# Optimization experiments

Hardware: AMD Instinct MI355X
Metric: run time of the kernel (lower is better)

The kernel has to match this reference:

```python
import jax, jax.numpy as jnp
import numpy as np

B, S, HID, H, D = 4, 1024, 2048, 16, 128
ROT = D // 2  # GLM 2D rotary: rotary dim is half the head dim (64)


def _rope_tables(seq_len, dim, base=10000.0):
    # dim = ROT; inv_freq over dim//2 frequencies, emb = cat(freqs, freqs)
    inv_freq = 1.0 / (base ** (jnp.arange(0, dim, 2, dtype=jnp.float32) / dim))
    t = jnp.arange(seq_len, dtype=jnp.float32)
    freqs = jnp.einsum('s,f->sf', t, inv_freq)          # [S, dim//2]
    emb = jnp.concatenate([freqs, freqs], axis=-1)       # [S, dim]
    return jnp.cos(emb), jnp.sin(emb)


def _rotate_half(x):
    x1, x2 = jnp.split(x, 2, axis=-1)
    return jnp.concatenate([-x2, x1], axis=-1)


def _apply_rope(x, cos, sin, pos_id):
    # x: [B,H,S,ROT]; pos_id: [B,S]; tables: [S,ROT]
    c = cos[pos_id][:, None, :, :]  # [B,1,S,ROT]
    s = sin[pos_id][:, None, :, :]
    return x * c + _rotate_half(x) * s


def setup_inputs() -> dict:
    key = jax.random.key(0)
    ks = jax.random.split(key, 12)
    w = 0.02
    inp = {
        'query': jax.random.normal(ks[0], (B, S, HID), jnp.float32),
        'key': jax.random.normal(ks[1], (B, S, HID), jnp.float32),
        'value': jax.random.normal(ks[2], (B, S, HID), jnp.float32),
        'mask': jnp.zeros((B, 1, S, S), jnp.float32),
        'position_bias': jax.random.normal(ks[3], (1, H, S, S), jnp.float32) * 0.1,
        'prev_attn': jax.random.normal(ks[4], (B, H, S, S), jnp.float32) * 0.1,
        'position_ids': jax.random.randint(ks[5], (B, 2, S), 0, S, jnp.int32),
        'Wq': jax.random.normal(ks[6], (HID, HID), jnp.float32) * w,
        'bq': jnp.zeros((HID,), jnp.float32),
        'Wk': jax.random.normal(ks[7], (HID, HID), jnp.float32) * w,
        'bk': jnp.zeros((HID,), jnp.float32),
        'Wv': jax.random.normal(ks[8], (HID, HID), jnp.float32) * w,
        'bv': jnp.zeros((HID,), jnp.float32),
        'Wo': jax.random.normal(ks[9], (HID, HID), jnp.float32) * w,
        'bo': jnp.zeros((HID,), jnp.float32),
    }
    return inp


def reference(query, key, value, mask, position_bias, prev_attn,
              Wq, bq, Wk, bk, Wv, bv, Wo, bo, position_ids):
    # QKV projections -> [B,H,S,D]
    def proj(x, W, b):
        return (x @ W.T + b).reshape(B, S, H, D).transpose(0, 2, 1, 3)
    q = proj(query, Wq, bq)
    k = proj(key, Wk, bk)
    v = proj(value, Wv, bv)

    # GLM 2D rotary: split head dim in halves, rope each with its own ids
    q1, q2 = jnp.split(q, 2, axis=-1)
    k1, k2 = jnp.split(k, 2, axis=-1)
    cos, sin = _rope_tables(S, ROT)
    pid = position_ids[:, 0, :]        # [B,S]
    bid = position_ids[:, 1, :]        # [B,S]
    q1 = _apply_rope(q1, cos, sin, pid)
    k1 = _apply_rope(k1, cos, sin, pid)
    q2 = _apply_rope(q2, cos, sin, bid)
    k2 = _apply_rope(k2, cos, sin, bid)
    q = jnp.concatenate([q1, q2], axis=-1)
    k = jnp.concatenate([k1, k2], axis=-1)

    scores = jnp.einsum('bhsd,bhtd->bhst', q, k)
    scores = scores + position_bias
    scores = scores / jnp.sqrt(jnp.float32(D))
    scores = scores + mask
    scores = scores + prev_attn          # residual attention accumulation
    prev_attn_out = scores
    probs = jax.nn.softmax(scores, axis=-1)
    ctx = jnp.einsum('bhst,bhtd->bhsd', probs, v)
    ctx = ctx.transpose(0, 2, 1, 3).reshape(B, S, HID)
    out = ctx @ Wo.T + bo
    return out, prev_attn_out
```

## Files before the change

kernel.cpp:

```cpp
#include <hip/hip_runtime.h>


#define B_  4
#define S_  1024
#define HID_ 2048
#define H_  16
#define D_  128
#define RSQRT_D 0.08838834764831845f

typedef _Float16 f16x8 __attribute__((ext_vector_type(8)));
typedef _Float16 f16x4 __attribute__((ext_vector_type(4)));
typedef float f32x4 __attribute__((ext_vector_type(4)));

#define MFMA16(a, b, c) __builtin_amdgcn_mfma_f32_16x16x32_f16(a, b, c, 0, 0, 0)

__device__ __forceinline__ void gll16(const void* g, void* l) {
  __builtin_amdgcn_global_load_lds(
      (const __attribute__((address_space(1))) void*)g,
      (__attribute__((address_space(3))) void*)l, 16, 0, 0);
}

__global__ __launch_bounds__(256) void cvt_all_kernel(
    const float* __restrict__ w0, const float* __restrict__ w1,
    const float* __restrict__ w2, const float* __restrict__ w3,
    const float* __restrict__ x0, const float* __restrict__ x1,
    const float* __restrict__ x2,
    _Float16* __restrict__ dw0, _Float16* __restrict__ dw1,
    _Float16* __restrict__ dw2, _Float16* __restrict__ dw3,
    _Float16* __restrict__ dx0, _Float16* __restrict__ dx1,
    _Float16* __restrict__ dx2,
    float* __restrict__ tcos, float* __restrict__ tsin) {
  if (blockIdx.x >= 20480) {
    const int i = (blockIdx.x - 20480) * 256 + threadIdx.x;
    const int pos = i >> 5, j = i & 31;
    const float inv = expf(-(float)j * (9.210340371976184f / 32.0f));
    const float ang = (float)pos * inv;
    tcos[i] = cosf(ang);
    tsin[i] = sinf(ang);
    return;
  }
  const int i = blockIdx.x * blockDim.x + threadIdx.x;
  const float* src;
  _Float16* dst;
  int off;
  if (i < 2097152) {
    const int seg = i >> 19;
    off = i & 524287;
    src = (seg == 0) ? w0 : (seg == 1) ? w1 : (seg == 2) ? w2 : w3;
    dst = (seg == 0) ? dw0 : (seg == 1) ? dw1 : (seg == 2) ? dw2 : dw3;
  } else {
    const int j = i - 2097152;
    const int seg = j >> 20;
    off = j & 1048575;
    src = (seg == 0) ? x0 : (seg == 1) ? x1 : x2;
    dst = (seg == 0) ? dx0 : (seg == 1) ? dx1 : dx2;
  }
  const f32x4* in4 = (const f32x4*)src;
  f32x4 a = in4[(size_t)off * 2], b = in4[(size_t)off * 2 + 1];
  f16x8 v;
  v[0] = (_Float16)a[0]; v[1] = (_Float16)a[1]; v[2] = (_Float16)a[2]; v[3] = (_Float16)a[3];
  v[4] = (_Float16)b[0]; v[5] = (_Float16)b[1]; v[6] = (_Float16)b[2]; v[7] = (_Float16)b[3];
  *(f16x8*)(dst + (size_t)off * 8) = v;
}

__global__ __launch_bounds__(256) void proj_qkv_kernel(
    const _Float16* __restrict__ Xq, const _Float16* __restrict__ Xk,
    const _Float16* __restrict__ Xv,
    const _Float16* __restrict__ Wq, const _Float16* __restrict__ Wk,
    const _Float16* __restrict__ Wv,
    const float* __restrict__ bq, const float* __restrict__ bk,
    const float* __restrict__ bv,
    _Float16* __restrict__ oq, _Float16* __restrict__ ok,
    _Float16* __restrict__ ovt,
    const int* __restrict__ pids, const float* __restrict__ tcos,
    const float* __restrict__ tsin) {
  constexpr int N = HID_, K = HID_;
  constexpr int BK = 64;
  __shared__ _Float16 As[128 * BK];
  __shared__ _Float16 Bs[128 * BK];

  const int tid = threadIdx.x;
  const int gbid = (blockIdx.x & 7) * 192 + (blockIdx.x >> 3);
  const int seg = gbid >> 9;
  const int bid = gbid & 511;
  const _Float16* A  = (seg == 0) ? Xq : (seg == 1) ? Xk : Xv;
  const _Float16* Bw = (seg == 0) ? Wq : (seg == 1) ? Wk : Wv;
  const float*  bias = (seg == 0) ? bq : (seg == 1) ? bk : bv;

  const int tm = bid >> 4, tn = bid & 15;
  const int m0 = tm * 128, n0 = tn * 128;
  const int w = tid >> 6, l = tid & 63;
  const int mw = (w >> 1) * 64, nw = (w & 1) * 64;
  const int lr = l & 15, lh = l >> 4;

  f32x4 acc[4][4] = {};

  for (int kt = 0; kt < K / BK; ++kt) {
    const int k0 = kt * BK;
    __syncthreads();
#pragma unroll
    for (int i = 0; i < 4; ++i) {
      const int e = i * 2048 + tid * 8;
      gll16(A + (size_t)(m0 + (e >> 6)) * K + k0 + (e & 63), As + e);
      gll16(Bw + (size_t)(n0 + (e >> 6)) * K + k0 + (e & 63), Bs + e);
    }
    asm volatile("s_waitcnt vmcnt(0)" ::: "memory");
    __syncthreads();
#pragma unroll
    for (int kk = 0; kk < 2; ++kk) {
      f16x8 af[4], bf[4];
#pragma unroll
      for (int mi = 0; mi < 4; ++mi)
        af[mi] = *(const f16x8*)(As + (mw + mi * 16 + lr) * BK + kk * 32 + lh * 8);
#pragma unroll
      for (int ni = 0; ni < 4; ++ni)
        bf[ni] = *(const f16x8*)(Bs + (nw + ni * 16 + lr) * BK + kk * 32 + lh * 8);
#pragma unroll
      for (int mi = 0; mi < 4; ++mi)
#pragma unroll
        for (int ni = 0; ni < 4; ++ni)
          acc[mi][ni] = MFMA16(af[mi], bf[ni], acc[mi][ni]);
    }
  }

  if (seg == 2) {
    _Float16* out = ovt;
#pragma unroll
    for (int mi = 0; mi < 4; ++mi)
#pragma unroll
      for (int ni = 0; ni < 4; ++ni) {
        const int col = n0 + nw + ni * 16 + lr;
        const float bb = bias[col];
        const int h = col >> 7, hd = col & 127;
#pragma unroll
        for (int r = 0; r < 4; ++r) {
          const int row = m0 + mw + mi * 16 + lh * 4 + r;
          const int b = row >> 10, s = row & 1023;
          out[(((size_t)(b * H_ + h)) * D_ + hd) * S_ + s] = (_Float16)(acc[mi][ni][r] + bb);
        }
      }
  } else {
    _Float16* out = (seg == 0) ? oq : ok;
    const int sel = (nw >> 6) & 1;
#pragma unroll
    for (int mi = 0; mi < 4; ++mi) {
#pragma unroll
      for (int r = 0; r < 4; ++r) {
        const int row = m0 + mw + mi * 16 + lh * 4 + r;
        const int b = row >> 10, s = row & 1023;
        const int pos = pids[b * 2 * S_ + sel * S_ + s];
#pragma unroll
        for (int ni = 0; ni < 2; ++ni) {
          const int col = n0 + nw + ni * 16 + lr;
          const int j = ni * 16 + lr;
          const float c = tcos[pos * 32 + j];
          const float sn = tsin[pos * 32 + j];
          const float x1 = acc[mi][ni][r] + bias[col];
          const float x2 = acc[mi][ni + 2][r] + bias[col + 32];
          const int h = col >> 7, hd = col & 127;
          const size_t base = (((size_t)(b * H_ + h)) * S_ + s) * D_;
          out[base + hd] = (_Float16)(x1 * c - x2 * sn);
          out[base + hd + 32] = (_Float16)(x2 * c + x1 * sn);
        }
      }
    }
  }
}

__global__ __launch_bounds__(256) void proj_out_kernel(
    const _Float16* __restrict__ A, const _Float16* __restrict__ Bw,
    const float* __restrict__ bias, float* __restrict__ out) {
  constexpr int N = HID_, K = HID_;
  constexpr int BK = 64;
  __shared__ _Float16 As[128 * BK];
  __shared__ _Float16 Bs[128 * BK];

  const int tid = threadIdx.x;
  const int bid = (blockIdx.x & 7) * 64 + (blockIdx.x >> 3);
  const int tm = bid >> 4, tn = bid & 15;
  const int m0 = tm * 128, n0 = tn * 128;
  const int w = tid >> 6, l = tid & 63;
  const int mw = (w >> 1) * 64, nw = (w & 1) * 64;
  const int lr = l & 15, lh = l >> 4;

  f32x4 acc[4][4] = {};

  for (int kt = 0; kt < K / BK; ++kt) {
    const int k0 = kt * BK;
    __syncthreads();
#pragma unroll
    for (int i = 0; i < 4; ++i) {
      const int e = i * 2048 + tid * 8;
      gll16(A + (size_t)(m0 + (e >> 6)) * K + k0 + (e & 63), As + e);
      gll16(Bw + (size_t)(n0 + (e >> 6)) * K + k0 + (e & 63), Bs + e);
    }
    asm volatile("s_waitcnt vmcnt(0)" ::: "memory");
    __syncthreads();
#pragma unroll
    for (int kk = 0; kk < 2; ++kk) {
      f16x8 af[4], bf[4];
#pragma unroll
      for (int mi = 0; mi < 4; ++mi)
        af[mi] = *(const f16x8*)(As + (mw + mi * 16 + lr) * BK + kk * 32 + lh * 8);
#pragma unroll
      for (int ni = 0; ni < 4; ++ni)
        bf[ni] = *(const f16x8*)(Bs + (nw + ni * 16 + lr) * BK + kk * 32 + lh * 8);
#pragma unroll
      for (int mi = 0; mi < 4; ++mi)
#pragma unroll
        for (int ni = 0; ni < 4; ++ni)
          acc[mi][ni] = MFMA16(af[mi], bf[ni], acc[mi][ni]);
    }
  }

#pragma unroll
  for (int mi = 0; mi < 4; ++mi)
#pragma unroll
    for (int ni = 0; ni < 4; ++ni) {
      const int col = n0 + nw + ni * 16 + lr;
      const float bb = bias[col];
#pragma unroll
      for (int r = 0; r < 4; ++r) {
        const int row = m0 + mw + mi * 16 + lh * 4 + r;
        out[(size_t)row * N + col] = acc[mi][ni][r] + bb;
      }
    }
}

__global__ __launch_bounds__(256) void flash_kernel(
    const _Float16* __restrict__ q, const _Float16* __restrict__ k,
    const _Float16* __restrict__ vt, const float* __restrict__ pbias,
    const float* __restrict__ maskp, const float* __restrict__ prev,
    float* __restrict__ scores, _Float16* __restrict__ ctx) {
  constexpr int BT = 64;
  __shared__ _Float16 KsBuf[2][BT * D_];
  __shared__ _Float16 VTsBuf[2][D_ * BT];
  __shared__ _Float16 Ps[4][16 * BT];

  const int tid = threadIdx.x, w = tid >> 6, l = tid & 63;
  const int lr = l & 15, lh = l >> 4;
  const int sid = (blockIdx.x & 7) * 128 + (blockIdx.x >> 3);
  const int qt = sid & 15, byh = sid >> 4;
  const int b = byh >> 4, h = byh & 15;
  const size_t plane = (size_t)byh;
  const int q0 = qt * 64 + w * 16;
  const int qrow = q0 + lr;
  const int swz = (lr & 7) << 3;

  const float* prow  = prev  + (plane * S_ + qrow) * S_;
  const float* pbrow = pbias + ((size_t)h * S_ + qrow) * S_;
  const float* mrow  = maskp + ((size_t)b * S_ + qrow) * S_;
  float*       srow  = scores + (plane * S_ + qrow) * S_;
  const _Float16* kpl = k  + plane * S_ * D_;
  const _Float16* vpl = vt + plane * D_ * S_;

  f16x8 qa[4];
#pragma unroll
  for (int kk = 0; kk < 4; ++kk)
    qa[kk] = *(const f16x8*)(q + (plane * S_ + qrow) * D_ + kk * 32 + lh * 8);

  f32x4 o[8] = {};
  float m_r = -1e30f, l_r = 0.0f;

  _Float16* ksA = &KsBuf[0][0];
  _Float16* ksB = &KsBuf[1][0];
  _Float16* vtA = &VTsBuf[0][0];
  _Float16* vtB = &VTsBuf[1][0];

#pragma unroll
  for (int i = 0; i < 4; ++i) {
    const int e = i * 2048 + tid * 8;
    const int krow = e >> 7;
    gll16(kpl + (size_t)krow * D_ + ((e & 127) ^ ((krow & 7) << 3)), ksA + e);
    const int vrow = e >> 6;
    gll16(vpl + (size_t)vrow * S_ + ((e & 63) ^ ((vrow & 7) << 3)), vtA + e);
  }
  __syncthreads();

  for (int tt = 0; tt < S_ / BT; ++tt) {
    const int t0 = tt * BT;

    f32x4 pv4[4], pb4[4], mk4[4];
#pragma unroll
    for (int nt = 0; nt < 4; ++nt) {
      const int toff = t0 + nt * 16 + lh * 4;
      pv4[nt] = __builtin_nontemporal_load((const f32x4*)(prow + toff));
      pb4[nt] = *(const f32x4*)(pbrow + toff);
      mk4[nt] = *(const f32x4*)(mrow + toff);
    }
    if (tt < S_ / BT - 1) {
      const int t1 = t0 + BT;
#pragma unroll
      for (int i = 0; i < 4; ++i) {
        const int e = i * 2048 + tid * 8;
        const int krow = e >> 7;
        gll16(kpl + (size_t)(t1 + krow) * D_ + ((e & 127) ^ ((krow & 7) << 3)), ksB + e);
        const int vrow = e >> 6;
        gll16(vpl + (size_t)vrow * S_ + t1 + ((e & 63) ^ ((vrow & 7) << 3)), vtB + e);
      }
    }

    f32x4 sa[4] = {};
    __builtin_amdgcn_s_setprio(1);
#pragma unroll
    for (int nt = 0; nt < 4; ++nt)
#pragma unroll
      for (int kk = 0; kk < 4; ++kk) {
        const int row = nt * 16 + lr;
        f16x8 kb = *(const f16x8*)(ksA + row * D_ + ((kk * 32 + lh * 8) ^ swz));
        sa[nt] = MFMA16(kb, qa[kk], sa[nt]);
      }
    __builtin_amdgcn_s_setprio(0);

#pragma unroll
    for (int nt = 0; nt < 4; ++nt) {
      const int toff = t0 + nt * 16 + lh * 4;
      f32x4 sc4 = (sa[nt] + pb4[nt]) * RSQRT_D + mk4[nt] + pv4[nt];
      __builtin_nontemporal_store(sc4, (f32x4*)(srow + toff));
      sa[nt] = sc4;
    }

    float tmx = -1e30f;
#pragma unroll
    for (int nt = 0; nt < 4; ++nt)
#pragma unroll
      for (int r = 0; r < 4; ++r) tmx = fmaxf(tmx, sa[nt][r]);
    tmx = fmaxf(tmx, __shfl_xor(tmx, 16));
    tmx = fmaxf(tmx, __shfl_xor(tmx, 32));
    if (!__all(tmx <= m_r + 8.0f)) {
      const float newm = fmaxf(m_r, tmx);
      const float al = __expf(m_r - newm);
      m_r = newm;
      l_r *= al;
#pragma unroll
      for (int nd = 0; nd < 8; ++nd) o[nd] *= al;
    }
    float ts = 0.0f;
#pragma unroll
    for (int nt = 0; nt < 4; ++nt)
#pragma unroll
      for (int r = 0; r < 4; ++r) {
        const float pe = __expf(sa[nt][r] - m_r);
        sa[nt][r] = pe;
        ts += pe;
      }
    ts += __shfl_xor(ts, 16);
    ts += __shfl_xor(ts, 32);
    l_r += ts;

    _Float16* pw = &Ps[w][0];
#pragma unroll
    for (int nt = 0; nt < 4; ++nt) {
      f16x4 pk;
      pk[0] = (_Float16)sa[nt][0]; pk[1] = (_Float16)sa[nt][1];
      pk[2] = (_Float16)sa[nt][2]; pk[3] = (_Float16)sa[nt][3];
      *(f16x4*)(pw + lr * BT + ((nt * 16 + lh * 4) ^ swz)) = pk;
    }

    __builtin_amdgcn_s_setprio(1);
#pragma unroll
    for (int kk2 = 0; kk2 < 2; ++kk2) {
      const f16x8 pa = *(const f16x8*)(pw + lr * BT + ((kk2 * 32 + lh * 8) ^ swz));
#pragma unroll
      for (int nd = 0; nd < 8; ++nd) {
        const int vr = nd * 16 + lr;
        const f16x8 vb = *(const f16x8*)(vtA + vr * BT + ((kk2 * 32 + lh * 8) ^ swz));
        o[nd] = MFMA16(vb, pa, o[nd]);
      }
    }
    __builtin_amdgcn_s_setprio(0);

    asm volatile("s_waitcnt vmcnt(4)" ::: "memory");
    __builtin_amdgcn_s_barrier();
    _Float16* t1p = ksA; ksA = ksB; ksB = t1p;
    _Float16* t2p = vtA; vtA = vtB; vtB = t2p;
  }

  const float inv_l = 1.0f / l_r;
  _Float16* crow = ctx + ((size_t)(b * S_) + qrow) * HID_ + h * D_;
#pragma unroll
  for (int nd = 0; nd < 8; ++nd) {
    f16x4 cv;
#pragma unroll
    for (int r = 0; r < 4; ++r) cv[r] = (_Float16)(o[nd][r] * inv_l);
    *(f16x4*)(crow + nd * 16 + lh * 4) = cv;
  }
}

extern "C" void kernel_launch(void* const* d_in, const int* in_sizes, int n_in,
                              void* d_out, int out_size, void* d_ws, size_t ws_size,
                              hipStream_t stream) {
  const float* query = (const float*)d_in[0];
  const float* key_i = (const float*)d_in[1];
  const float* value = (const float*)d_in[2];
  const float* maskp = (const float*)d_in[3];
  const float* pbias = (const float*)d_in[4];
  const float* prev  = (const float*)d_in[5];
  const int*   pids  = (const int*)d_in[6];
  const float* Wq = (const float*)d_in[7];
  const float* bq = (const float*)d_in[8];
  const float* Wk = (const float*)d_in[9];
  const float* bk = (const float*)d_in[10];
  const float* Wv = (const float*)d_in[11];
  const float* bv = (const float*)d_in[12];
  const float* Wo = (const float*)d_in[13];
  const float* bo = (const float*)d_in[14];

  char* ws = (char*)d_ws;
  const size_t OFF_TCOS = 0;
  const size_t OFF_TSIN = 131072;
  const size_t OFF_W    = 262144;
  const size_t OFF_X    = OFF_W + 4ull * 8388608;
  const size_t OFF_Q    = OFF_X + 3ull * 16777216;
  const size_t OFF_K    = OFF_Q + 16777216;
  const size_t OFF_VT   = OFF_K + 16777216;
  const size_t OFF_CTX  = OFF_X + 16777216;

  float* tcos = (float*)(ws + OFF_TCOS);
  float* tsin = (float*)(ws + OFF_TSIN);
  _Float16* Wq16 = (_Float16*)(ws + OFF_W);
  _Float16* Wk16 = (_Float16*)(ws + OFF_W + 8388608);
  _Float16* Wv16 = (_Float16*)(ws + OFF_W + 2ull * 8388608);
  _Float16* Wo16 = (_Float16*)(ws + OFF_W + 3ull * 8388608);
  _Float16* Xq16 = (_Float16*)(ws + OFF_X);
  _Float16* Xk16 = (_Float16*)(ws + OFF_X + 16777216);
  _Float16* Xv16 = (_Float16*)(ws + OFF_X + 2ull * 16777216);
  _Float16* q16  = (_Float16*)(ws + OFF_Q);
  _Float16* k16  = (_Float16*)(ws + OFF_K);
  _Float16* vt16 = (_Float16*)(ws + OFF_VT);
  _Float16* ctx16 = (_Float16*)(ws + OFF_CTX);

  float* out_f32 = (float*)d_out;
  float* scores  = (float*)d_out + 8388608;

  cvt_all_kernel<<<20608, 256, 0, stream>>>(Wq, Wk, Wv, Wo, query, key_i, value,
                                            Wq16, Wk16, Wv16, Wo16,
                                            Xq16, Xk16, Xv16, tcos, tsin);

  proj_qkv_kernel<<<1536, 256, 0, stream>>>(Xq16, Xk16, Xv16,
                                            Wq16, Wk16, Wv16,
                                            bq, bk, bv,
                                            q16, k16, vt16,
                                            pids, tcos, tsin);

  flash_kernel<<<1024, 256, 0, stream>>>(q16, k16, vt16, pbias, maskp, prev,
                                         scores, ctx16);

  proj_out_kernel<<<512, 256, 0, stream>>>(ctx16, Wo16, bo, out_f32);
}
```

Before: 445.3 us.

## Single-buffer K/V tiles and pass P through lane shuffles instead of LDS

```diff
diff --git a/kernel.cpp b/kernel.cpp
--- a/kernel.cpp
+++ b/kernel.cpp
@@ -11,6 +11,8 @@
 typedef _Float16 f16x8 __attribute__((ext_vector_type(8)));
 typedef _Float16 f16x4 __attribute__((ext_vector_type(4)));
 typedef float f32x4 __attribute__((ext_vector_type(4)));
+typedef unsigned int u32x2 __attribute__((ext_vector_type(2)));
+typedef unsigned int u32x4 __attribute__((ext_vector_type(4)));
 
 #define MFMA16(a, b, c) __builtin_amdgcn_mfma_f32_16x16x32_f16(a, b, c, 0, 0, 0)
 
@@ -233,9 +235,8 @@
     const float* __restrict__ maskp, const float* __restrict__ prev,
     float* __restrict__ scores, _Float16* __restrict__ ctx) {
   constexpr int BT = 64;
-  __shared__ _Float16 KsBuf[2][BT * D_];
-  __shared__ _Float16 VTsBuf[2][D_ * BT];
-  __shared__ _Float16 Ps[4][16 * BT];
+  __shared__ _Float16 Ks[BT * D_];
+  __shared__ _Float16 VTs[D_ * BT];
 
   const int tid = threadIdx.x, w = tid >> 6, l = tid & 63;
   const int lr = l & 15, lh = l >> 4;
@@ -247,6 +248,10 @@
   const int qrow = q0 + lr;
   const int swz = (lr & 7) << 3;
 
+  const int srcA = lr + ((l & 16) << 1);
+  const int srcB = srcA + 16;
+  const bool selHi = (l & 32) != 0;
+
   const float* prow  = prev  + (plane * S_ + qrow) * S_;
   const float* pbrow = pbias + ((size_t)h * S_ + qrow) * S_;
   const float* mrow  = maskp + ((size_t)b * S_ + qrow) * S_;
@@ -262,21 +267,6 @@
   f32x4 o[8] = {};
   float m_r = -1e30f, l_r = 0.0f;
 
-  _Float16* ksA = &KsBuf[0][0];
-  _Float16* ksB = &KsBuf[1][0];
-  _Float16* vtA = &VTsBuf[0][0];
-  _Float16* vtB = &VTsBuf[1][0];
-
-#pragma unroll
-  for (int i = 0; i < 4; ++i) {
-    const int e = i * 2048 + tid * 8;
-    const int krow = e >> 7;
-    gll16(kpl + (size_t)krow * D_ + ((e & 127) ^ ((krow & 7) << 3)), ksA + e);
-    const int vrow = e >> 6;
-    gll16(vpl + (size_t)vrow * S_ + ((e & 63) ^ ((vrow & 7) << 3)), vtA + e);
-  }
-  __syncthreads();
-
   for (int tt = 0; tt < S_ / BT; ++tt) {
     const int t0 = tt * BT;
 
@@ -284,21 +274,19 @@
 #pragma unroll
     for (int nt = 0; nt < 4; ++nt) {
       const int toff = t0 + nt * 16 + lh * 4;
-      pv4[nt] = __builtin_nontemporal_load((const f32x4*)(prow + toff));
+      pv4[nt] = *(const f32x4*)(prow + toff);
       pb4[nt] = *(const f32x4*)(pbrow + toff);
       mk4[nt] = *(const f32x4*)(mrow + toff);
     }
-    if (tt < S_ / BT - 1) {
-      const int t1 = t0 + BT;
-#pragma unroll
-      for (int i = 0; i < 4; ++i) {
-        const int e = i * 2048 + tid * 8;
-        const int krow = e >> 7;
-        gll16(kpl + (size_t)(t1 + krow) * D_ + ((e & 127) ^ ((krow & 7) << 3)), ksB + e);
-        const int vrow = e >> 6;
-        gll16(vpl + (size_t)vrow * S_ + t1 + ((e & 63) ^ ((vrow & 7) << 3)), vtB + e);
-      }
-    }
+#pragma unroll
+    for (int i = 0; i < 4; ++i) {
+      const int e = i * 2048 + tid * 8;
+      const int krow = e >> 7;
+      gll16(kpl + (size_t)(t0 + krow) * D_ + ((e & 127) ^ ((krow & 7) << 3)), Ks + e);
+      const int vrow = e >> 6;
+      gll16(vpl + (size_t)vrow * S_ + t0 + ((e & 63) ^ ((vrow & 7) << 3)), VTs + e);
+    }
+    __syncthreads();
 
     f32x4 sa[4] = {};
     __builtin_amdgcn_s_setprio(1);
@@ -307,7 +295,7 @@
 #pragma unroll
       for (int kk = 0; kk < 4; ++kk) {
         const int row = nt * 16 + lr;
-        f16x8 kb = *(const f16x8*)(ksA + row * D_ + ((kk * 32 + lh * 8) ^ swz));
+        f16x8 kb = *(const f16x8*)(Ks + row * D_ + ((kk * 32 + lh * 8) ^ swz));
         sa[nt] = MFMA16(kb, qa[kk], sa[nt]);
       }
     __builtin_amdgcn_s_setprio(0);
@@ -316,7 +304,7 @@
     for (int nt = 0; nt < 4; ++nt) {
       const int toff = t0 + nt * 16 + lh * 4;
       f32x4 sc4 = (sa[nt] + pb4[nt]) * RSQRT_D + mk4[nt] + pv4[nt];
-      __builtin_nontemporal_store(sc4, (f32x4*)(srow + toff));
+      *(f32x4*)(srow + toff) = sc4;
       sa[nt] = sc4;
     }
 
@@ -348,32 +336,51 @@
     ts += __shfl_xor(ts, 32);
     l_r += ts;
 
-    _Float16* pw = &Ps[w][0];
-#pragma unroll
-    for (int nt = 0; nt < 4; ++nt) {
-      f16x4 pk;
-      pk[0] = (_Float16)sa[nt][0]; pk[1] = (_Float16)sa[nt][1];
-      pk[2] = (_Float16)sa[nt][2]; pk[3] = (_Float16)sa[nt][3];
-      *(f16x4*)(pw + lr * BT + ((nt * 16 + lh * 4) ^ swz)) = pk;
-    }
+    unsigned int u0w0, u0w1, u1w0, u1w1, u2w0, u2w1, u3w0, u3w1;
+    {
+      f16x4 pk0, pk1, pk2, pk3;
+#pragma unroll
+      for (int r = 0; r < 4; ++r) {
+        pk0[r] = (_Float16)sa[0][r]; pk1[r] = (_Float16)sa[1][r];
+        pk2[r] = (_Float16)sa[2][r]; pk3[r] = (_Float16)sa[3][r];
+      }
+      u32x2 v0 = __builtin_bit_cast(u32x2, pk0); u0w0 = v0[0]; u0w1 = v0[1];
+      u32x2 v1 = __builtin_bit_cast(u32x2, pk1); u1w0 = v1[0]; u1w1 = v1[1];
+      u32x2 v2 = __builtin_bit_cast(u32x2, pk2); u2w0 = v2[0]; u2w1 = v2[1];
+      u32x2 v3 = __builtin_bit_cast(u32x2, pk3); u3w0 = v3[0]; u3w1 = v3[1];
+    }
+    const unsigned a00 = (unsigned)__shfl((int)u0w0, srcA), a01 = (unsigned)__shfl((int)u0w1, srcA);
+    const unsigned a10 = (unsigned)__shfl((int)u1w0, srcA), a11 = (unsigned)__shfl((int)u1w1, srcA);
+    const unsigned a20 = (unsigned)__shfl((int)u2w0, srcA), a21 = (unsigned)__shfl((int)u2w1, srcA);
+    const unsigned a30 = (unsigned)__shfl((int)u3w0, srcA), a31 = (unsigned)__shfl((int)u3w1, srcA);
+    const unsigned b00 = (unsigned)__shfl((int)u0w0, srcB), b01 = (unsigned)__shfl((int)u0w1, srcB);
+    const unsigned b10 = (unsigned)__shfl((int)u1w0, srcB), b11 = (unsigned)__shfl((int)u1w1, srcB);
+    const unsigned b20 = (unsigned)__shfl((int)u2w0, srcB), b21 = (unsigned)__shfl((int)u2w1, srcB);
+    const unsigned b30 = (unsigned)__shfl((int)u3w0, srcB), b31 = (unsigned)__shfl((int)u3w1, srcB);
+    u32x4 paw0, paw1;
+    paw0[0] = selHi ? a10 : a00; paw0[1] = selHi ? a11 : a01;
+    paw0[2] = selHi ? b10 : b00; paw0[3] = selHi ? b11 : b01;
+    paw1[0] = selHi ? a30 : a20; paw1[1] = selHi ? a31 : a21;
+    paw1[2] = selHi ? b30 : b20; paw1[3] = selHi ? b31 : b21;
+    const f16x8 pa0 = __builtin_bit_cast(f16x8, paw0);
+    const f16x8 pa1 = __builtin_bit_cast(f16x8, paw1);
 
     __builtin_amdgcn_s_setprio(1);
 #pragma unroll
-    for (int kk2 = 0; kk2 < 2; ++kk2) {
-      const f16x8 pa = *(const f16x8*)(pw + lr * BT + ((kk2 * 32 + lh * 8) ^ swz));
-#pragma unroll
-      for (int nd = 0; nd < 8; ++nd) {
-        const int vr = nd * 16 + lr;
-        const f16x8 vb = *(const f16x8*)(vtA + vr * BT + ((kk2 * 32 + lh * 8) ^ swz));
-        o[nd] = MFMA16(vb, pa, o[nd]);
-      }
+    for (int nd = 0; nd < 8; ++nd) {
+      const int vr = nd * 16 + lr;
+      const f16x8 vb0 = *(const f16x8*)(VTs + vr * BT + ((lh * 8) ^ swz));
+      o[nd] = MFMA16(vb0, pa0, o[nd]);
+    }
+#pragma unroll
+    for (int nd = 0; nd < 8; ++nd) {
+      const int vr = nd * 16 + lr;
+      const f16x8 vb1 = *(const f16x8*)(VTs + vr * BT + ((32 + lh * 8) ^ swz));
+      o[nd] = MFMA16(vb1, pa1, o[nd]);
     }
     __builtin_amdgcn_s_setprio(0);
 
-    asm volatile("s_waitcnt vmcnt(4)" ::: "memory");
     __builtin_amdgcn_s_barrier();
-    _Float16* t1p = ksA; ksA = ksB; ksB = t1p;
-    _Float16* t2p = vtA; vtA = vtB; vtB = t2p;
   }
 
   const float inv_l = 1.0f / l_r;
```

Result: slower. 474.1 us (+6.5%).

## Restructure QKV projection GEMM into 256x256 double-buffered tiles with swizzled LDS

Applied to the files above, without the earlier changes.

```diff
diff --git a/kernel.cpp b/kernel.cpp
--- a/kernel.cpp
+++ b/kernel.cpp
@@ -63,7 +63,20 @@
   *(f16x8*)(dst + (size_t)off * 8) = v;
 }
 
-__global__ __launch_bounds__(256) void proj_qkv_kernel(
+__device__ __forceinline__ void stage_tile_256(
+    const _Float16* __restrict__ A, const _Float16* __restrict__ Bw,
+    int m0, int n0, int k0s, _Float16* ad, _Float16* bd, int tid) {
+#pragma unroll
+  for (int i = 0; i < 4; ++i) {
+    const int e = i * 4096 + tid * 8;
+    const int rrow = e >> 6;
+    const int rcol = (e & 63) ^ ((rrow & 7) << 3);
+    gll16(A + (size_t)(m0 + rrow) * HID_ + k0s + rcol, ad + e);
+    gll16(Bw + (size_t)(n0 + rrow) * HID_ + k0s + rcol, bd + e);
+  }
+}
+
+__global__ __launch_bounds__(512) void proj_qkv_kernel(
     const _Float16* __restrict__ Xq, const _Float16* __restrict__ Xk,
     const _Float16* __restrict__ Xv,
     const _Float16* __restrict__ Wq, const _Float16* __restrict__ Wk,
@@ -74,87 +87,103 @@
     _Float16* __restrict__ ovt,
     const int* __restrict__ pids, const float* __restrict__ tcos,
     const float* __restrict__ tsin) {
-  constexpr int N = HID_, K = HID_;
+  constexpr int K = HID_;
   constexpr int BK = 64;
-  __shared__ _Float16 As[128 * BK];
-  __shared__ _Float16 Bs[128 * BK];
+  constexpr int NK = K / BK;
+  __shared__ _Float16 As[2][256 * BK];
+  __shared__ _Float16 Bs[2][256 * BK];
 
   const int tid = threadIdx.x;
-  const int gbid = (blockIdx.x & 7) * 192 + (blockIdx.x >> 3);
-  const int seg = gbid >> 9;
-  const int bid = gbid & 511;
+  const int gbid = (blockIdx.x & 7) * 48 + (blockIdx.x >> 3);
+  const int seg = gbid / 128;
+  const int bid = gbid % 128;
   const _Float16* A  = (seg == 0) ? Xq : (seg == 1) ? Xk : Xv;
   const _Float16* Bw = (seg == 0) ? Wq : (seg == 1) ? Wk : Wv;
   const float*  bias = (seg == 0) ? bq : (seg == 1) ? bk : bv;
 
-  const int tm = bid >> 4, tn = bid & 15;
-  const int m0 = tm * 128, n0 = tn * 128;
+  const int tm = bid >> 3, tn = bid & 7;
+  const int m0 = tm * 256, n0 = tn * 256;
   const int w = tid >> 6, l = tid & 63;
-  const int mw = (w >> 1) * 64, nw = (w & 1) * 64;
+  const int wr = w >> 2, wc = w & 3;
   const int lr = l & 15, lh = l >> 4;
-
-  f32x4 acc[4][4] = {};
-
-  for (int kt = 0; kt < K / BK; ++kt) {
-    const int k0 = kt * BK;
-    __syncthreads();
-#pragma unroll
-    for (int i = 0; i < 4; ++i) {
-      const int e = i * 2048 + tid * 8;
-      gll16(A + (size_t)(m0 + (e >> 6)) * K + k0 + (e & 63), As + e);
-      gll16(Bw + (size_t)(n0 + (e >> 6)) * K + k0 + (e & 63), Bs + e);
-    }
-    asm volatile("s_waitcnt vmcnt(0)" ::: "memory");
-    __syncthreads();
-#pragma unroll
-    for (int kk = 0; kk < 2; ++kk) {
+  const int swz = (lr & 7) << 3;
+
+  f32x4 acc[8][4] = {};
+
+  stage_tile_256(A, Bw, m0, n0, 0, &As[0][0], &Bs[0][0], tid);
+
+  for (int j = 0; j < NK; ++j) {
+    const _Float16* as = &As[j & 1][0];
+    const _Float16* bs = &Bs[j & 1][0];
+
+    if (j + 1 < NK) {
+      stage_tile_256(A, Bw, m0, n0, (j + 1) * BK,
+                     &As[(j + 1) & 1][0], &Bs[(j + 1) & 1][0], tid);
+      asm volatile("s_waitcnt vmcnt(8)" ::: "memory");
+    } else {
+      asm volatile("s_waitcnt vmcnt(0)" ::: "memory");
+    }
+    __builtin_amdgcn_sched_barrier(0);
+    __builtin_amdgcn_s_barrier();
+
+#pragma unroll
+    for (int p = 0; p < 4; ++p) {
+      const int qm = p & 1, kk = p >> 1;
+      if (p > 0) __builtin_amdgcn_s_barrier();
       f16x8 af[4], bf[4];
 #pragma unroll
-      for (int mi = 0; mi < 4; ++mi)
-        af[mi] = *(const f16x8*)(As + (mw + mi * 16 + lr) * BK + kk * 32 + lh * 8);
+      for (int i = 0; i < 4; ++i)
+        af[i] = *(const f16x8*)(as + (wr * 128 + (qm * 4 + i) * 16 + lr) * BK +
+                                ((kk * 32 + lh * 8) ^ swz));
 #pragma unroll
       for (int ni = 0; ni < 4; ++ni)
-        bf[ni] = *(const f16x8*)(Bs + (nw + ni * 16 + lr) * BK + kk * 32 + lh * 8);
-#pragma unroll
-      for (int mi = 0; mi < 4; ++mi)
+        bf[ni] = *(const f16x8*)(bs + (wc * 64 + ni * 16 + lr) * BK +
+                                 ((kk * 32 + lh * 8) ^ swz));
+      asm volatile("s_waitcnt lgkmcnt(0)" ::: "memory");
+      __builtin_amdgcn_sched_barrier(0);
+      __builtin_amdgcn_s_setprio(1);
+#pragma unroll
+      for (int i = 0; i < 4; ++i)
 #pragma unroll
         for (int ni = 0; ni < 4; ++ni)
-          acc[mi][ni] = MFMA16(af[mi], bf[ni], acc[mi][ni]);
-    }
+          acc[qm * 4 + i][ni] = MFMA16(af[i], bf[ni], acc[qm * 4 + i][ni]);
+      __builtin_amdgcn_s_setprio(0);
+    }
+    __builtin_amdgcn_s_barrier();
   }
 
   if (seg == 2) {
-    _Float16* out = ovt;
-#pragma unroll
-    for (int mi = 0; mi < 4; ++mi)
+#pragma unroll
+    for (int mi = 0; mi < 8; ++mi)
 #pragma unroll
       for (int ni = 0; ni < 4; ++ni) {
-        const int col = n0 + nw + ni * 16 + lr;
+        const int col = n0 + wc * 64 + ni * 16 + lr;
         const float bb = bias[col];
         const int h = col >> 7, hd = col & 127;
 #pragma unroll
         for (int r = 0; r < 4; ++r) {
-          const int row = m0 + mw + mi * 16 + lh * 4 + r;
+          const int row = m0 + wr * 128 + mi * 16 + lh * 4 + r;
           const int b = row >> 10, s = row & 1023;
-          out[(((size_t)(b * H_ + h)) * D_ + hd) * S_ + s] = (_Float16)(acc[mi][ni][r] + bb);
+          ovt[(((size_t)(b * H_ + h)) * D_ + hd) * S_ + s] =
+              (_Float16)(acc[mi][ni][r] + bb);
         }
       }
   } else {
     _Float16* out = (seg == 0) ? oq : ok;
-    const int sel = (nw >> 6) & 1;
-#pragma unroll
-    for (int mi = 0; mi < 4; ++mi) {
+    const int sel = wc & 1;
+#pragma unroll
+    for (int mi = 0; mi < 8; ++mi) {
 #pragma unroll
       for (int r = 0; r < 4; ++r) {
-        const int row = m0 + mw + mi * 16 + lh * 4 + r;
+        const int row = m0 + wr * 128 + mi * 16 + lh * 4 + r;
         const int b = row >> 10, s = row & 1023;
         const int pos = pids[b * 2 * S_ + sel * S_ + s];
 #pragma unroll
         for (int ni = 0; ni < 2; ++ni) {
-          const int col = n0 + nw + ni * 16 + lr;
-          const int j = ni * 16 + lr;
-          const float c = tcos[pos * 32 + j];
-          const float sn = tsin[pos * 32 + j];
+          const int col = n0 + wc * 64 + ni * 16 + lr;
+          const int jf = ni * 16 + lr;
+          const float c = tcos[pos * 32 + jf];
+          const float sn = tsin[pos * 32 + jf];
           const float x1 = acc[mi][ni][r] + bias[col];
           const float x2 = acc[mi][ni + 2][r] + bias[col + 32];
           const int h = col >> 7, hd = col & 127;
@@ -437,11 +466,11 @@
                                             Wq16, Wk16, Wv16, Wo16,
                                             Xq16, Xk16, Xv16, tcos, tsin);
 
-  proj_qkv_kernel<<<1536, 256, 0, stream>>>(Xq16, Xk16, Xv16,
-                                            Wq16, Wk16, Wv16,
-                                            bq, bk, bv,
-                                            q16, k16, vt16,
-                                            pids, tcos, tsin);
+  proj_qkv_kernel<<<384, 512, 0, stream>>>(Xq16, Xk16, Xv16,
+                                           Wq16, Wk16, Wv16,
+                                           bq, bk, bv,
+                                           q16, k16, vt16,
+                                           pids, tcos, tsin);
 
   flash_kernel<<<1024, 256, 0, stream>>>(q16, k16, vt16, pbias, maskp, prev,
                                          scores, ctx16);
```

Result: no change. 444.1 us, median of 2 (-0.3%).
